# Performance work log

Hardware: AMD Instinct MI355X
Metric: run time of the kernel (lower is better)

Reference implementation:

```python
import jax, jax.numpy as jnp
import numpy as np

B, N_KV, N_Q = 32, 4096, 8
D_INP, D_SLOT, HEADS, MLP_H = 256, 256, 4, 1024
ITERS = 3
EPS = 1e-8


def _ln(x, g, b, eps=1e-5):
    m = jnp.mean(x, axis=-1, keepdims=True)
    v = jnp.var(x, axis=-1, keepdims=True)
    return (x - m) * jax.lax.rsqrt(v + eps) * g + b


def setup_inputs() -> dict:
    key = jax.random.key(0)
    ks = jax.random.split(key, 12)
    def w(k, shape, fan_in):
        return jax.random.normal(k, shape, jnp.float32) / np.float32(np.sqrt(fan_in))
    return {
        "inputs": jax.random.normal(ks[0], (B, N_KV, D_INP), jnp.float32),
        "slots": jax.random.normal(ks[1], (B, N_Q, D_SLOT), jnp.float32),
        "ln_in_g": jnp.ones((D_INP,), jnp.float32), "ln_in_b": jnp.zeros((D_INP,), jnp.float32),
        "ln_slot_g": jnp.ones((D_SLOT,), jnp.float32), "ln_slot_b": jnp.zeros((D_SLOT,), jnp.float32),
        "ln_mlp_g": jnp.ones((D_SLOT,), jnp.float32), "ln_mlp_b": jnp.zeros((D_SLOT,), jnp.float32),
        "Wq": w(ks[2], (D_SLOT, D_SLOT), D_SLOT),
        "Wk": w(ks[3], (D_SLOT, D_INP), D_INP),
        "Wv": w(ks[4], (D_SLOT, D_INP), D_INP),
        "W_ih": w(ks[5], (3 * D_SLOT, D_SLOT), D_SLOT),
        "W_hh": w(ks[6], (3 * D_SLOT, D_SLOT), D_SLOT),
        "b_ih": jnp.zeros((3 * D_SLOT,), jnp.float32),
        "b_hh": jnp.zeros((3 * D_SLOT,), jnp.float32),
        "W1": w(ks[7], (MLP_H, D_SLOT), D_SLOT), "b1": jnp.zeros((MLP_H,), jnp.float32),
        "W2": w(ks[8], (D_SLOT, MLP_H), MLP_H), "b2": jnp.zeros((D_SLOT,), jnp.float32),
    }


def reference(inputs, slots, ln_in_g, ln_in_b, ln_slot_g, ln_slot_b, ln_mlp_g, ln_mlp_b,
              Wq, Wk, Wv, W_ih, W_hh, b_ih, b_hh, W1, b1, W2, b2):
    Bb, Nkv, _ = inputs.shape
    _, Nq, Ds = slots.shape
    hd = Ds // HEADS

    x = _ln(inputs, ln_in_g, ln_in_b)
    # k, v: [B, H, N_kv, hd]; k pre-scaled by hd**-0.5 as in the original
    k = (x @ Wk.T).reshape(Bb, Nkv, HEADS, hd).transpose(0, 2, 1, 3) * (hd ** -0.5)
    v = (x @ Wv.T).reshape(Bb, Nkv, HEADS, hd).transpose(0, 2, 1, 3)

    attn_vis = attn_temp = None
    for it in range(ITERS):
        if it == ITERS - 1:
            slots = jax.lax.stop_gradient(slots)
        slots_prev = slots
        s = _ln(slots, ln_slot_g, ln_slot_b)
        q = (s @ Wq.T).reshape(Bb, Nq, HEADS, hd).transpose(0, 2, 1, 3)  # [B,H,Nq,hd]
        logits = jnp.einsum('bhnd,bhqd->bhnq', k, q)  # [B,H,Nkv,Nq]
        # competing softmax: normalize jointly over (head, slot) per input token
        lt = logits.transpose(0, 2, 1, 3).reshape(Bb, Nkv, HEADS * Nq)
        attn = jax.nn.softmax(lt, axis=-1).reshape(Bb, Nkv, HEADS, Nq).transpose(0, 2, 1, 3)
        attn_vis = attn.sum(axis=1)   # [B, Nkv, Nq]
        attn_temp = attn_vis          # original recomputes the identical softmax; same values
        a = attn + EPS
        a = a / a.sum(axis=-2, keepdims=True)  # renormalize over N_kv
        updates = jnp.einsum('bhnq,bhnd->bhqd', a, v).transpose(0, 2, 1, 3).reshape(Bb, Nq, Ds)
        # GRU cell (torch GRUCell math)
        gx = updates @ W_ih.T + b_ih
        gh = slots_prev @ W_hh.T + b_hh
        xr, xz, xn = jnp.split(gx, 3, axis=-1)
        hr, hz, hn = jnp.split(gh, 3, axis=-1)
        r = jax.nn.sigmoid(xr + hr)
        z = jax.nn.sigmoid(xz + hz)
        n = jnp.tanh(xn + r * hn)
        slots = (1.0 - z) * n + z * slots_prev
        # MLP with residual
        m = _ln(slots, ln_mlp_g, ln_mlp_b)
        slots = slots + (jax.nn.relu(m @ W1.T + b1) @ W2.T + b2)
    return slots, attn_vis, attn_temp
```

## Files before the change

kernel.cpp:

```cpp
#include <hip/hip_runtime.h>
#include <math.h>


#define NKV   4096
#define DD    256
#define HQN   32
#define EPSR  1e-8f

#define WS_V      0
#define WS_A0     262144
#define WS_A1     263168
#define WS_C0     264192
#define WS_C1     265216
#define WS_SLOTA  266240
#define WS_SLOTB  331776
#define WS_WQT    397312
#define WS_QF     462848
#define WS_WPGXH  528384
#define WS_WFT    921600
#define WS_WHHT   1314816
#define WS_W1T    1413120
#define WS_W2T    1544192
#define WS_RS     1675264
#define WS_RM     1806336
#define WS_VPART  1937408

typedef float f32x4 __attribute__((ext_vector_type(4)));
typedef short s16x8 __attribute__((ext_vector_type(8)));
typedef int   v2i   __attribute__((ext_vector_type(2)));

__device__ __forceinline__ unsigned bfr(float f) {
    unsigned u = __float_as_uint(f);
    return (u + 0x7fffu + ((u >> 16) & 1u)) >> 16;
}
__device__ __forceinline__ unsigned pk2(float lo, float hi) {
    return bfr(lo) | (bfr(hi) << 16);
}
__device__ __forceinline__ float bf2f(unsigned short us) {
    return __uint_as_float((unsigned)us << 16);
}
__device__ __forceinline__ float bflo(unsigned u) { return __uint_as_float(u << 16); }
__device__ __forceinline__ float bfhi(unsigned u) { return __uint_as_float(u & 0xffff0000u); }

__device__ __forceinline__ v2i tr_read(unsigned addr) {
    v2i d;
    asm volatile("ds_read_b64_tr_b16 %0, %1" : "=v"(d) : "v"(addr));
    return d;
}
__device__ __forceinline__ s16x8 mk_frag(v2i a, v2i b) {
    union { int i[4]; s16x8 s; } u;
    u.i[0] = a.x; u.i[1] = a.y; u.i[2] = b.x; u.i[3] = b.y;
    return u.s;
}

__global__ __launch_bounds__(256) void k_copy(const float* __restrict__ in,
                                              float* __restrict__ out, int n) {
    int i = blockIdx.x * 256 + threadIdx.x;
    if (i < n) out[i] = in[i];
}

__global__ __launch_bounds__(256) void k_tr(const float* __restrict__ in,
                                            float* __restrict__ out, int R, int C) {
    __shared__ float tile[32][33];
    int bx = blockIdx.x * 32, by = blockIdx.y * 32;
    int x = bx + threadIdx.x;
    for (int k = 0; k < 32; k += 8) {
        int y = by + threadIdx.y + k;
        if (x < C && y < R) tile[threadIdx.y + k][threadIdx.x] = in[(size_t)y * C + x];
    }
    __syncthreads();
    int r = by + threadIdx.x;
    for (int k = 0; k < 32; k += 8) {
        int c = bx + threadIdx.y + k;
        if (c < C && r < R) out[(size_t)c * R + r] = tile[threadIdx.x][threadIdx.y + k];
    }
}

__global__ __launch_bounds__(256) void k_wfold(
    const float* __restrict__ Wih, const float* __restrict__ Wv,
    unsigned* __restrict__ WfT2)
{
    __shared__ float wr[256];
    const int c = blockIdx.x, t = threadIdx.x;
    wr[t] = Wih[(size_t)c * 256 + t];
    __syncthreads();
    const float2* wv2 = (const float2*)Wv;
    #pragma unroll
    for (int pp = 0; pp < 2; ++pp) {
        int P = pp * 256 + t;
        int h = P >> 7, p = P & 127;
        float f0 = 0.f, f1 = 0.f;
        #pragma unroll 8
        for (int d = 0; d < 64; ++d) {
            float a = wr[h * 64 + d];
            float2 v = wv2[(size_t)(h * 64 + d) * 128 + p];
            f0 = fmaf(a, v.x, f0); f1 = fmaf(a, v.y, f1);
        }
        WfT2[(size_t)P * 768 + c] = pk2(f0, f1);
    }
}

__global__ __launch_bounds__(256) void k_trpack(
    const float* __restrict__ in, unsigned* __restrict__ out, int R, int C)
{
    const int c2 = blockIdx.x;
    const int t = threadIdx.x;
    for (int q = 0; q < R / 256; ++q) {
        int r = q * 256 + t;
        out[(size_t)c2 * R + r] = pk2(in[(size_t)r * C + 2 * c2],
                                      in[(size_t)r * C + 2 * c2 + 1]);
    }
}

__global__ __launch_bounds__(256) void k_prep_a(
    const float* __restrict__ slots, const float* __restrict__ g_s, const float* __restrict__ b_s,
    const float* __restrict__ wqt, float* __restrict__ qf_g,
    float* __restrict__ A0_g, float* __restrict__ A1_g)
{
    __shared__ float s_row[256];
    __shared__ float red[8];
    const int t = threadIdx.x;
    const int b = blockIdx.x, qi = blockIdx.y;
    const int lane = t & 63, w = t >> 6;

    if (t < 4) { A0_g[b * 32 + t * 8 + qi] = 0.f; A1_g[b * 32 + t * 8 + qi] = 0.f; }

    float v = slots[((size_t)b * 8 + qi) * 256 + t];
    float s0 = v, s1 = v * v;
    #pragma unroll
    for (int o = 32; o >= 1; o >>= 1) { s0 += __shfl_xor(s0, o, 64); s1 += __shfl_xor(s1, o, 64); }
    if (lane == 0) { red[w] = s0; red[4 + w] = s1; }
    __syncthreads();
    {
        float m = (red[0] + red[1] + red[2] + red[3]) * (1.f / 256.f);
        float q2 = (red[4] + red[5] + red[6] + red[7]) * (1.f / 256.f);
        float rs = rsqrtf(q2 - m * m + 1e-5f);
        s_row[t] = (v - m) * rs * g_s[t] + b_s[t];
    }
    __syncthreads();

    float a = 0.f;
    #pragma unroll 8
    for (int j = 0; j < 256; ++j)
        a = fmaf(s_row[j], wqt[j * 256 + t], a);
    qf_g[((size_t)b * 8 + qi) * 256 + t] = a;
}

__global__ __launch_bounds__(256) void k_prep_b(
    const float* __restrict__ qf_g, const float* __restrict__ Wk,
    const float* __restrict__ g_in, const float* __restrict__ b_in,
    unsigned short* __restrict__ wp_bf, float* __restrict__ c0_g, float* __restrict__ c1_g)
{
    __shared__ float qs[512];
    __shared__ float redc[4096];
    const int t = threadIdx.x;
    const int b = blockIdx.x, h = blockIdx.y;
    const int lane = t & 63, w = t >> 6;
    const float LNS = 0.125f * 1.44269504f;

    #pragma unroll
    for (int rep = 0; rep < 2; ++rep) {
        int idx = rep * 256 + t;
        int qi = idx >> 6, d = idx & 63;
        qs[idx] = qf_g[((size_t)b * 8 + qi) * 256 + h * 64 + d];
    }
    __syncthreads();

    float a2[8];
    #pragma unroll
    for (int qi = 0; qi < 8; ++qi) a2[qi] = 0.f;
    #pragma unroll 4
    for (int d = 0; d < 64; ++d) {
        float wv = Wk[(size_t)(h * 64 + d) * 256 + t];
        #pragma unroll
        for (int qi = 0; qi < 8; ++qi) a2[qi] = fmaf(qs[qi * 64 + d], wv, a2[qi]);
    }
    const float gv = g_in[t], bv = b_in[t];
    #pragma unroll
    for (int qi = 0; qi < 8; ++qi) {
        float kv = LNS * a2[qi];
        float we = kv * gv;
        wp_bf[((size_t)b * HQN + h * 8 + qi) * 256 + t] = (unsigned short)bfr(we);
        redc[qi * 256 + t] = we;
        redc[2048 + qi * 256 + t] = kv * bv;
    }
    __syncthreads();
    #pragma unroll
    for (int rep = 0; rep < 2; ++rep) {
        int r = w * 2 + rep;
        float sv1 = redc[r * 256 + lane] + redc[r * 256 + 64 + lane] +
                    redc[r * 256 + 128 + lane] + redc[r * 256 + 192 + lane];
        float sv0 = redc[2048 + r * 256 + lane] + redc[2048 + r * 256 + 64 + lane] +
                    redc[2048 + r * 256 + 128 + lane] + redc[2048 + r * 256 + 192 + lane];
        #pragma unroll
        for (int o = 32; o >= 1; o >>= 1) {
            sv1 += __shfl_xor(sv1, o, 64);
            sv0 += __shfl_xor(sv0, o, 64);
        }
        if (lane == 0) {
            c1_g[b * 32 + h * 8 + r] = sv1;
            c0_g[b * 32 + h * 8 + r] = sv0;
        }
    }
}

__device__ __forceinline__ void load_x(const float* __restrict__ inp, int b, int n0,
                                       int tok_s, int seg8, float4* ld) {
    const float4* row4 = (const float4*)(inp + ((size_t)b * NKV + n0 + tok_s) * 256);
    #pragma unroll
    for (int u = 0; u < 8; ++u) ld[u] = row4[(u >> 2) * 32 + seg8 * 4 + (u & 3)];
}

__device__ __forceinline__ void pack_x(const float4* ld, char* dst, int tok_s, int seg8) {
    #pragma unroll
    for (int c = 0; c < 2; ++c) {
        int nt = seg8 + 8 * c;
        #pragma unroll
        for (int h = 0; h < 2; ++h) {
            float4 fa = ld[c * 4 + h * 2], fb = ld[c * 4 + h * 2 + 1];
            uint4 pk;
            pk.x = pk2(fa.x, fa.y); pk.y = pk2(fa.z, fa.w);
            pk.z = pk2(fb.x, fb.y); pk.w = pk2(fb.z, fb.w);
            *(uint4*)(dst + nt * 1040 + tok_s * 32 + h * 16) = pk;
        }
    }
}

__device__ __forceinline__ void calc_stats(const float4* ld, float* sb,
                                           float* __restrict__ rs_g, float* __restrict__ rm_g,
                                           int b, int n0, int tok_s, int seg8) {
    float s0 = 0.f, s1 = 0.f;
    #pragma unroll
    for (int u = 0; u < 8; ++u) {
        float4 v = ld[u];
        s0 += v.x + v.y + v.z + v.w;
        s1 = fmaf(v.x, v.x, s1); s1 = fmaf(v.y, v.y, s1);
        s1 = fmaf(v.z, v.z, s1); s1 = fmaf(v.w, v.w, s1);
    }
    s0 += __shfl_xor(s0, 1, 64); s1 += __shfl_xor(s1, 1, 64);
    s0 += __shfl_xor(s0, 2, 64); s1 += __shfl_xor(s1, 2, 64);
    s0 += __shfl_xor(s0, 4, 64); s1 += __shfl_xor(s1, 4, 64);
    float m  = s0 * (1.f / 256.f);
    float rs = rsqrtf(s1 * (1.f / 256.f) - m * m + 1e-5f);
    if (seg8 == 0) {
        sb[tok_s] = rs;
        sb[32 + tok_s] = rs * m;
        rs_g[b * 4096 + n0 + tok_s] = rs;
        rm_g[b * 4096 + n0 + tok_s] = rs * m;
    }
}

template<int NC, int STATS, int WVIS>
__global__ __launch_bounds__(256) void k_attn(
    const float* __restrict__ inp, const unsigned short* __restrict__ wp_bf,
    const float* __restrict__ c0_g, const float* __restrict__ c1_g,
    float* __restrict__ vpart, float* __restrict__ A0_g, float* __restrict__ A1_g,
    float* __restrict__ rs_g, float* __restrict__ rm_g,
    float* __restrict__ out_vis, float* __restrict__ out_temp)
{
    constexpr int KBMAX = 128 / NC;
    __shared__ unsigned short xb[2][8320];
    __shared__ unsigned short wl[8192];
    __shared__ unsigned short pt[1024];
    __shared__ float stats[2][64];
    __shared__ float redm[64];
    __shared__ float reds[64];

    const int t = threadIdx.x;
    const int l = t & 63, w = t >> 6;
    const int g = l >> 4, li = l & 15;
    const int b = blockIdx.y, kb = blockIdx.x;

    char* xbB = (char*)xb;
    char* wlB = (char*)wl;
    char* ptB = (char*)pt;
    const int tok_s = t >> 3, seg8 = t & 7;
    const int cbase = kb * NC;

    {
        const uint4* wp4 = (const uint4*)wp_bf + ((size_t)b * 8192 + (t >> 3) * 256 + (t & 7) * 32) / 8;
        const int hq = t >> 3, sg = t & 7;
        #pragma unroll
        for (int q = 0; q < 4; ++q) {
            uint4 v = wp4[q];
            *(uint4*)(wlB + hq * 512 + (((sg * 4 + q) ^ (hq & 7)) * 16)) = v;
        }
    }

    const int Mt = w & 1, Nt = w >> 1;
    const int hqB = Nt * 16 + li;
    const float c0r = c0_g[b * 32 + hqB];
    const float c1r = c1_g[b * 32 + hqB];
    const int MtV = w >> 1, ntb = (w & 1) * 8;
    const int hqA = MtV * 16 + li;

    f32x4 av[8];
    #pragma unroll
    for (int u = 0; u < 8; ++u) av[u] = (f32x4){0.f, 0.f, 0.f, 0.f};
    float A0acc = 0.f, A1acc = 0.f;

    const unsigned xbase = (unsigned)(uintptr_t)xbB;

    {
        float4 ldA[8];
        load_x(inp, b, cbase * 32, tok_s, seg8, ldA);
        if (STATS) {
            calc_stats(ldA, &stats[0][0], rs_g, rm_g, b, cbase * 32, tok_s, seg8);
        } else {
            if (t < 32) stats[0][t] = rs_g[b * 4096 + cbase * 32 + t];
            else if (t < 64) stats[0][t] = rm_g[b * 4096 + cbase * 32 + t - 32];
        }
        pack_x(ldA, xbB, tok_s, seg8);
    }
    __syncthreads();

    #pragma unroll
    for (int ci = 0; ci < NC; ++ci) {
        const int cur = ci & 1, nxt = cur ^ 1;
        const int n0 = (cbase + ci) * 32;
        char* xc = xbB + cur * 16640;
        char* xn = xbB + nxt * 16640;

        float4 ldN[8];
        if (ci < NC - 1) load_x(inp, b, n0 + 32, tok_s, seg8, ldN);
        __builtin_amdgcn_sched_barrier(0);

        f32x4 accS = (f32x4){0.f, 0.f, 0.f, 0.f};
        #pragma unroll
        for (int kk = 0; kk < 8; ++kk) {
            s16x8 af = *(const s16x8*)(xc + (kk * 2 + (g >> 1)) * 1040 +
                                       (Mt * 16 + li) * 32 + (g & 1) * 16);
            s16x8 bf = *(const s16x8*)(wlB + hqB * 512 + (((kk * 4 + g) ^ (hqB & 7)) * 16));
            accS = __builtin_amdgcn_mfma_f32_16x16x32_bf16(af, bf, accS, 0, 0, 0);
        }

        float lg[4], rsv[4], rmv[4], mh[4], ex[4], aa[4];
        #pragma unroll
        for (int r = 0; r < 4; ++r) {
            int tokr = Mt * 16 + g * 4 + r;
            rsv[r] = stats[cur][tokr];
            rmv[r] = stats[cur][32 + tokr];
            lg[r] = fmaf(rsv[r], accS[r], fmaf(-rmv[r], c1r, c0r));
        }
        #pragma unroll
        for (int r = 0; r < 4; ++r) {
            float v = lg[r];
            v = fmaxf(v, __shfl_xor(v, 1, 64));
            v = fmaxf(v, __shfl_xor(v, 2, 64));
            v = fmaxf(v, __shfl_xor(v, 4, 64));
            v = fmaxf(v, __shfl_xor(v, 8, 64));
            mh[r] = v;
            ex[r] = exp2f(lg[r] - v);
            float s = ex[r];
            s += __shfl_xor(s, 1, 64);
            s += __shfl_xor(s, 2, 64);
            s += __shfl_xor(s, 4, 64);
            s += __shfl_xor(s, 8, 64);
            if (li == 0) {
                int tokr = Mt * 16 + g * 4 + r;
                redm[tokr * 2 + Nt] = v;
                reds[tokr * 2 + Nt] = s;
            }
        }
        __syncthreads();
        #pragma unroll
        for (int r = 0; r < 4; ++r) {
            int tokr = Mt * 16 + g * 4 + r;
            float m0 = redm[tokr * 2], m1 = redm[tokr * 2 + 1];
            float mx = fmaxf(m0, m1);
            float tot = reds[tokr * 2] * exp2f(m0 - mx) + reds[tokr * 2 + 1] * exp2f(m1 - mx);
            aa[r] = ex[r] * (exp2f(mh[r] - mx) / tot);
            A0acc += aa[r];
            A1acc = fmaf(aa[r], rmv[r], A1acc);
        }
        {
            uint2 pw;
            pw.x = pk2(aa[0] * rsv[0], aa[1] * rsv[1]);
            pw.y = pk2(aa[2] * rsv[2], aa[3] * rsv[3]);
            int tokb = Mt * 16 + g * 4;
            int slot = (tokb >> 3) ^ ((hqB >> 1) & 3);
            *(uint2*)(ptB + hqB * 64 + slot * 16 + (tokb & 7) * 2) = pw;
        }
        __syncthreads();

        if (WVIS) {
            int tk = t >> 3, q = t & 7;
            float sv = 0.f;
            #pragma unroll
            for (int h = 0; h < 4; ++h) {
                int hq = h * 8 + q;
                int slot = (tk >> 3) ^ ((hq >> 1) & 3);
                sv += bf2f(*(const unsigned short*)(ptB + hq * 64 + slot * 16 + (tk & 7) * 2));
            }
            float vv = sv / stats[cur][tk];
            size_t o = ((size_t)b * NKV + n0 + tk) * 8 + q;
            out_vis[o] = vv; out_temp[o] = vv;
        }

        if (ci < NC - 1) {
            if (STATS) {
                calc_stats(ldN, &stats[nxt][0], rs_g, rm_g, b, n0 + 32, tok_s, seg8);
            } else {
                if (t < 32) stats[nxt][t] = rs_g[b * 4096 + n0 + 32 + t];
                else if (t < 64) stats[nxt][t] = rm_g[b * 4096 + n0 + 32 + t - 32];
            }
            pack_x(ldN, xn, tok_s, seg8);
        }

        {
            s16x8 pa = *(const s16x8*)(ptB + hqA * 64 + ((g ^ ((hqA >> 1) & 3)) * 16));
            unsigned abase = xbase + cur * 16640 + g * 256 + li * 8;
            v2i t0a = tr_read(abase + (ntb + 0) * 1040);
            v2i t0b = tr_read(abase + (ntb + 0) * 1040 + 128);
            v2i t1a = tr_read(abase + (ntb + 1) * 1040);
            v2i t1b = tr_read(abase + (ntb + 1) * 1040 + 128);
            v2i t2a = tr_read(abase + (ntb + 2) * 1040);
            v2i t2b = tr_read(abase + (ntb + 2) * 1040 + 128);
            v2i t3a = tr_read(abase + (ntb + 3) * 1040);
            v2i t3b = tr_read(abase + (ntb + 3) * 1040 + 128);
            asm volatile("s_waitcnt lgkmcnt(0)" ::: "memory");
            __builtin_amdgcn_sched_barrier(0);
            av[0] = __builtin_amdgcn_mfma_f32_16x16x32_bf16(pa, mk_frag(t0a, t0b), av[0], 0, 0, 0);
            av[1] = __builtin_amdgcn_mfma_f32_16x16x32_bf16(pa, mk_frag(t1a, t1b), av[1], 0, 0, 0);
            av[2] = __builtin_amdgcn_mfma_f32_16x16x32_bf16(pa, mk_frag(t2a, t2b), av[2], 0, 0, 0);
            av[3] = __builtin_amdgcn_mfma_f32_16x16x32_bf16(pa, mk_frag(t3a, t3b), av[3], 0, 0, 0);
            v2i t4a = tr_read(abase + (ntb + 4) * 1040);
            v2i t4b = tr_read(abase + (ntb + 4) * 1040 + 128);
            v2i t5a = tr_read(abase + (ntb + 5) * 1040);
            v2i t5b = tr_read(abase + (ntb + 5) * 1040 + 128);
            v2i t6a = tr_read(abase + (ntb + 6) * 1040);
            v2i t6b = tr_read(abase + (ntb + 6) * 1040 + 128);
            v2i t7a = tr_read(abase + (ntb + 7) * 1040);
            v2i t7b = tr_read(abase + (ntb + 7) * 1040 + 128);
            asm volatile("s_waitcnt lgkmcnt(0)" ::: "memory");
            __builtin_amdgcn_sched_barrier(0);
            av[4] = __builtin_amdgcn_mfma_f32_16x16x32_bf16(pa, mk_frag(t4a, t4b), av[4], 0, 0, 0);
            av[5] = __builtin_amdgcn_mfma_f32_16x16x32_bf16(pa, mk_frag(t5a, t5b), av[5], 0, 0, 0);
            av[6] = __builtin_amdgcn_mfma_f32_16x16x32_bf16(pa, mk_frag(t6a, t6b), av[6], 0, 0, 0);
            av[7] = __builtin_amdgcn_mfma_f32_16x16x32_bf16(pa, mk_frag(t7a, t7b), av[7], 0, 0, 0);
        }
        __syncthreads();
    }

    A0acc += __shfl_xor(A0acc, 16, 64); A0acc += __shfl_xor(A0acc, 32, 64);
    A1acc += __shfl_xor(A1acc, 16, 64); A1acc += __shfl_xor(A1acc, 32, 64);
    if (g == 0) {
        atomicAdd(A0_g + b * 32 + hqB, A0acc);
        atomicAdd(A1_g + b * 32 + hqB, A1acc);
    }
    float* vp = vpart + ((size_t)(b * KBMAX + kb) * 32) * 256;
    #pragma unroll
    for (int i = 0; i < 8; ++i) {
        int j = (ntb + i) * 16 + li;
        #pragma unroll
        for (int r = 0; r < 4; ++r) {
            int hq = MtV * 16 + g * 4 + r;
            vp[(size_t)hq * 256 + j] = av[i][r];
        }
    }
}

template<int KBMAX>
__global__ __launch_bounds__(256) void k_vred(
    const float* __restrict__ vpart, float* __restrict__ V_g)
{
    const int t = threadIdx.x;
    const int b = blockIdx.x, hq = blockIdx.y;
    const float* p = vpart + ((size_t)(b * KBMAX) * 32 + hq) * 256 + t;
    float s = 0.f;
    #pragma unroll 8
    for (int kb = 0; kb < KBMAX; ++kb)
        s += p[(size_t)kb * 8192];
    V_g[((size_t)b * 32 + hq) * 256 + t] = s;
}

__global__ __launch_bounds__(256) void k_gates(
    const float* __restrict__ V_g, const float* __restrict__ A0_g,
    const float* __restrict__ A1_g,
    const float* __restrict__ g_in, const float* __restrict__ b_in,
    const float* __restrict__ slot_cur,
    const unsigned* __restrict__ WfT2, const unsigned* __restrict__ WhhT2,
    float* __restrict__ gxh, float* __restrict__ slot_nxt,
    float* __restrict__ out_slots)
{
    __shared__ __align__(16) float aT[1024 * 4];
    const int t = threadIdx.x;
    const int rg = blockIdx.y;
    const int chunk = blockIdx.x;
    const int row0 = rg * 4;
    float acc0 = 0.f, acc1 = 0.f, acc2 = 0.f, acc3 = 0.f;

    if (chunk == 0) {
        #pragma unroll
        for (int rr = 0; rr < 4; ++rr) {
            slot_nxt[(size_t)(row0 + rr) * 256 + t] = 0.f;
            if (out_slots) out_slots[(size_t)(row0 + rr) * 256 + t] = 0.f;
        }
    }

    if (chunk < 3) {
        const int b = rg >> 1, qi0 = (rg & 1) * 4;
        const float gt = g_in[t], bt = b_in[t];
        #pragma unroll
        for (int kk = 0; kk < 4; ++kk) {
            float4 y4;
            #pragma unroll
            for (int rr = 0; rr < 4; ++rr) {
                int hq = kk * 8 + qi0 + rr;
                float A0 = A0_g[b * 32 + hq], A1 = A1_g[b * 32 + hq];
                float den = A0 + EPSR * (float)NKV;
                float vv = V_g[((size_t)b * 32 + hq) * 256 + t];
                float yv = (gt * (vv - A1) + bt * A0) / den;
                ((float*)&y4)[rr] = yv;
            }
            *(float4*)(aT + (kk * 256 + t) * 4) = y4;
        }
        __syncthreads();
        const unsigned* wp = WfT2 + chunk * 256 + t;
        #pragma unroll 4
        for (int k2 = 0; k2 < 512; ++k2) {
            unsigned wv = wp[(size_t)k2 * 768];
            float w0 = bflo(wv), w1 = bfhi(wv);
            float4 a0 = *(const float4*)(aT + 8 * k2);
            float4 a1 = *(const float4*)(aT + 8 * k2 + 4);
            acc0 = fmaf(a0.x, w0, acc0); acc0 = fmaf(a1.x, w1, acc0);
            acc1 = fmaf(a0.y, w0, acc1); acc1 = fmaf(a1.y, w1, acc1);
            acc2 = fmaf(a0.z, w0, acc2); acc2 = fmaf(a1.z, w1, acc2);
            acc3 = fmaf(a0.w, w0, acc3); acc3 = fmaf(a1.w, w1, acc3);
        }
        float* go = gxh + (size_t)row0 * 1536 + chunk * 256 + t;
        go[0] = acc0; go[1536] = acc1; go[3072] = acc2; go[4608] = acc3;
    } else {
        const int gc = chunk - 3;
        {
            float4 y4;
            #pragma unroll
            for (int rr = 0; rr < 4; ++rr)
                ((float*)&y4)[rr] = slot_cur[(size_t)(row0 + rr) * 256 + t];
            *(float4*)(aT + t * 4) = y4;
        }
        __syncthreads();
        const unsigned* wp = WhhT2 + gc * 256 + t;
        #pragma unroll 4
        for (int k2 = 0; k2 < 128; ++k2) {
            unsigned wv = wp[(size_t)k2 * 768];
            float w0 = bflo(wv), w1 = bfhi(wv);
            float4 a0 = *(const float4*)(aT + 8 * k2);
            float4 a1 = *(const float4*)(aT + 8 * k2 + 4);
            acc0 = fmaf(a0.x, w0, acc0); acc0 = fmaf(a1.x, w1, acc0);
            acc1 = fmaf(a0.y, w0, acc1); acc1 = fmaf(a1.y, w1, acc1);
            acc2 = fmaf(a0.z, w0, acc2); acc2 = fmaf(a1.z, w1, acc2);
            acc3 = fmaf(a0.w, w0, acc3); acc3 = fmaf(a1.w, w1, acc3);
        }
        float* go = gxh + (size_t)row0 * 1536 + 768 + gc * 256 + t;
        go[0] = acc0; go[1536] = acc1; go[3072] = acc2; go[4608] = acc3;
    }
}

__global__ __launch_bounds__(256) void k_mlp(
    const float* __restrict__ gxh, const float* __restrict__ slot_cur,
    const float* __restrict__ bih, const float* __restrict__ bhh,
    const float* __restrict__ gm, const float* __restrict__ bm,
    const unsigned* __restrict__ W1T2, const float* __restrict__ b1,
    const unsigned* __restrict__ W2T2, const float* __restrict__ b2,
    float* __restrict__ slot_nxt, float* __restrict__ out_slots)
{
    __shared__ __align__(16) float mT[1024];
    __shared__ float sm_l[4][256];
    __shared__ float h1_l[4][256];
    __shared__ float lnst[8];
    const int t = threadIdx.x;
    const int rg = blockIdx.y, chunk = blockIdx.x;
    const int row0 = rg * 4;
    const int lane = t & 63, w = t >> 6;

    const float bi0 = bih[t], bi1 = bih[256 + t], bi2 = bih[512 + t];
    const float bh0 = bhh[t], bh1 = bhh[256 + t], bh2 = bhh[512 + t];
    float smid[4];
    #pragma unroll
    for (int rr = 0; rr < 4; ++rr) {
        const float* gr = gxh + (size_t)(row0 + rr) * 1536;
        float gx0 = gr[t], gx1 = gr[256 + t], gx2 = gr[512 + t];
        float gh0 = gr[768 + t], gh1 = gr[1024 + t], gh2 = gr[1280 + t];
        float spv = slot_cur[(size_t)(row0 + rr) * 256 + t];
        float r = 1.f / (1.f + __expf(-(gx0 + bi0 + gh0 + bh0)));
        float z = 1.f / (1.f + __expf(-(gx1 + bi1 + gh1 + bh1)));
        float n = tanhf(gx2 + bi2 + r * (gh2 + bh2));
        smid[rr] = (1.f - z) * n + z * spv;
        sm_l[rr][t] = smid[rr];
    }
    __syncthreads();
    {
        float4 v = *(const float4*)(&sm_l[w][lane * 4]);
        float s0 = v.x + v.y + v.z + v.w;
        float s1 = v.x * v.x + v.y * v.y + v.z * v.z + v.w * v.w;
        #pragma unroll
        for (int o = 32; o >= 1; o >>= 1) { s0 += __shfl_xor(s0, o, 64); s1 += __shfl_xor(s1, o, 64); }
        if (lane == 0) {
            float mu = s0 * (1.f / 256.f);
            lnst[w * 2] = mu;
            lnst[w * 2 + 1] = rsqrtf(s1 * (1.f / 256.f) - mu * mu + 1e-5f);
        }
    }
    __syncthreads();
    {
        const float gmt = gm[t], bmt = bm[t];
        float4 m4;
        #pragma unroll
        for (int rr = 0; rr < 4; ++rr)
            ((float*)&m4)[rr] = (smid[rr] - lnst[rr * 2]) * lnst[rr * 2 + 1] * gmt + bmt;
        *(float4*)(mT + t * 4) = m4;
    }
    __syncthreads();

    {
        float acc0 = 0.f, acc1 = 0.f, acc2 = 0.f, acc3 = 0.f;
        const unsigned* wp = W1T2 + chunk * 256 + t;
        #pragma unroll 4
        for (int k2 = 0; k2 < 128; ++k2) {
            unsigned wv = wp[(size_t)k2 * 1024];
            float w0 = bflo(wv), w1 = bfhi(wv);
            float4 a0 = *(const float4*)(mT + 8 * k2);
            float4 a1 = *(const float4*)(mT + 8 * k2 + 4);
            acc0 = fmaf(a0.x, w0, acc0); acc0 = fmaf(a1.x, w1, acc0);
            acc1 = fmaf(a0.y, w0, acc1); acc1 = fmaf(a1.y, w1, acc1);
            acc2 = fmaf(a0.z, w0, acc2); acc2 = fmaf(a1.z, w1, acc2);
            acc3 = fmaf(a0.w, w0, acc3); acc3 = fmaf(a1.w, w1, acc3);
        }
        const float b1t = b1[chunk * 256 + t];
        h1_l[0][t] = fmaxf(acc0 + b1t, 0.f);
        h1_l[1][t] = fmaxf(acc1 + b1t, 0.f);
        h1_l[2][t] = fmaxf(acc2 + b1t, 0.f);
        h1_l[3][t] = fmaxf(acc3 + b1t, 0.f);
    }
    __syncthreads();

    {
        float o0 = 0.f, o1 = 0.f, o2 = 0.f, o3 = 0.f;
        const unsigned* wp = W2T2 + (size_t)(chunk * 128) * 256 + t;
        #pragma unroll 4
        for (int k2 = 0; k2 < 128; ++k2) {
            unsigned wv = wp[(size_t)k2 * 256];
            float w0 = bflo(wv), w1 = bfhi(wv);
            float a00 = h1_l[0][2 * k2], a01 = h1_l[0][2 * k2 + 1];
            float a10 = h1_l[1][2 * k2], a11 = h1_l[1][2 * k2 + 1];
            float a20 = h1_l[2][2 * k2], a21 = h1_l[2][2 * k2 + 1];
            float a30 = h1_l[3][2 * k2], a31 = h1_l[3][2 * k2 + 1];
            o0 = fmaf(a00, w0, o0); o0 = fmaf(a01, w1, o0);
            o1 = fmaf(a10, w0, o1); o1 = fmaf(a11, w1, o1);
            o2 = fmaf(a20, w0, o2); o2 = fmaf(a21, w1, o2);
            o3 = fmaf(a30, w0, o3); o3 = fmaf(a31, w1, o3);
        }
        const float b2t = b2[t];
        float p0 = o0 + ((chunk == 0) ? smid[0] + b2t : 0.f);
        float p1 = o1 + ((chunk == 0) ? smid[1] + b2t : 0.f);
        float p2 = o2 + ((chunk == 0) ? smid[2] + b2t : 0.f);
        float p3 = o3 + ((chunk == 0) ? smid[3] + b2t : 0.f);
        atomicAdd(slot_nxt + (size_t)(row0 + 0) * 256 + t, p0);
        atomicAdd(slot_nxt + (size_t)(row0 + 1) * 256 + t, p1);
        atomicAdd(slot_nxt + (size_t)(row0 + 2) * 256 + t, p2);
        atomicAdd(slot_nxt + (size_t)(row0 + 3) * 256 + t, p3);
        if (out_slots) {
            atomicAdd(out_slots + (size_t)(row0 + 0) * 256 + t, p0);
            atomicAdd(out_slots + (size_t)(row0 + 1) * 256 + t, p1);
            atomicAdd(out_slots + (size_t)(row0 + 2) * 256 + t, p2);
            atomicAdd(out_slots + (size_t)(row0 + 3) * 256 + t, p3);
        }
    }
}

extern "C" void kernel_launch(void* const* d_in, const int* in_sizes, int n_in,
                              void* d_out, int out_size, void* d_ws, size_t ws_size,
                              hipStream_t stream) {
    const float* inp     = (const float*)d_in[0];
    const float* slots0  = (const float*)d_in[1];
    const float* ln_in_g = (const float*)d_in[2];
    const float* ln_in_b = (const float*)d_in[3];
    const float* ln_s_g  = (const float*)d_in[4];
    const float* ln_s_b  = (const float*)d_in[5];
    const float* ln_m_g  = (const float*)d_in[6];
    const float* ln_m_b  = (const float*)d_in[7];
    const float* Wq  = (const float*)d_in[8];
    const float* Wk  = (const float*)d_in[9];
    const float* Wv  = (const float*)d_in[10];
    const float* Wih = (const float*)d_in[11];
    const float* Whh = (const float*)d_in[12];
    const float* bih = (const float*)d_in[13];
    const float* bhh = (const float*)d_in[14];
    const float* W1  = (const float*)d_in[15];
    const float* b1  = (const float*)d_in[16];
    const float* W2  = (const float*)d_in[17];
    const float* b2  = (const float*)d_in[18];

    float* ws = (float*)d_ws;
    float* V_g   = ws + WS_V;
    float* A0_g  = ws + WS_A0;
    float* A1_g  = ws + WS_A1;
    float* c0_g  = ws + WS_C0;
    float* c1_g  = ws + WS_C1;
    float* slotA = ws + WS_SLOTA;
    float* slotB = ws + WS_SLOTB;
    float* wqt   = ws + WS_WQT;
    float* qf_g  = ws + WS_QF;
    float* gxh   = ws + WS_WPGXH;
    unsigned short* wp_bf = (unsigned short*)(ws + WS_WPGXH);
    unsigned* WfT2  = (unsigned*)(ws + WS_WFT);
    unsigned* WhhT2 = (unsigned*)(ws + WS_WHHT);
    unsigned* W1T2  = (unsigned*)(ws + WS_W1T);
    unsigned* W2T2  = (unsigned*)(ws + WS_W2T);
    float* rs_g  = ws + WS_RS;
    float* rm_g  = ws + WS_RM;
    float* vpart = ws + WS_VPART;

    const int useNC2 = (ws_size >= (size_t)(WS_VPART + 32ull * 64 * 8192) * 4) ? 1 : 0;

    float* out_slots = (float*)d_out;
    float* out_vis   = out_slots + 32 * 8 * 256;
    float* out_temp  = out_vis + 32 * 4096 * 8;

    k_tr<<<dim3(8, 8), dim3(32, 8), 0, stream>>>(Wq, wqt, 256, 256);
    k_wfold<<<768, 256, 0, stream>>>(Wih, Wv, WfT2);
    k_trpack<<<128, 256, 0, stream>>>(Whh, WhhT2, 768, 256);
    k_trpack<<<128, 256, 0, stream>>>(W1, W1T2, 1024, 256);
    k_trpack<<<512, 256, 0, stream>>>(W2, W2T2, 256, 1024);
    k_copy<<<256, 256, 0, stream>>>(slots0, slotA, 65536);

    for (int it = 0; it < 3; ++it) {
        float* cur = (it & 1) ? slotB : slotA;
        float* nxt = (it & 1) ? slotA : slotB;
        k_prep_a<<<dim3(32, 8), 256, 0, stream>>>(cur, ln_s_g, ln_s_b, wqt, qf_g,
                                                  A0_g, A1_g);
        k_prep_b<<<dim3(32, 4), 256, 0, stream>>>(qf_g, Wk, ln_in_g, ln_in_b,
                                                  wp_bf, c0_g, c1_g);
        if (useNC2) {
            if (it == 0)
                k_attn<2, 1, 0><<<dim3(64, 32), 256, 0, stream>>>(
                    inp, wp_bf, c0_g, c1_g, vpart, A0_g, A1_g, rs_g, rm_g, out_vis, out_temp);
            else if (it == 1)
                k_attn<2, 0, 0><<<dim3(64, 32), 256, 0, stream>>>(
                    inp, wp_bf, c0_g, c1_g, vpart, A0_g, A1_g, rs_g, rm_g, out_vis, out_temp);
            else
                k_attn<2, 0, 1><<<dim3(64, 32), 256, 0, stream>>>(
                    inp, wp_bf, c0_g, c1_g, vpart, A0_g, A1_g, rs_g, rm_g, out_vis, out_temp);
            k_vred<64><<<dim3(32, 32), 256, 0, stream>>>(vpart, V_g);
        } else {
            if (it == 0)
                k_attn<4, 1, 0><<<dim3(32, 32), 256, 0, stream>>>(
                    inp, wp_bf, c0_g, c1_g, vpart, A0_g, A1_g, rs_g, rm_g, out_vis, out_temp);
            else if (it == 1)
                k_attn<4, 0, 0><<<dim3(32, 32), 256, 0, stream>>>(
                    inp, wp_bf, c0_g, c1_g, vpart, A0_g, A1_g, rs_g, rm_g, out_vis, out_temp);
            else
                k_attn<4, 0, 1><<<dim3(32, 32), 256, 0, stream>>>(
                    inp, wp_bf, c0_g, c1_g, vpart, A0_g, A1_g, rs_g, rm_g, out_vis, out_temp);
            k_vred<32><<<dim3(32, 32), 256, 0, stream>>>(vpart, V_g);
        }
        k_gates<<<dim3(6, 64), 256, 0, stream>>>(
            V_g, A0_g, A1_g, ln_in_g, ln_in_b, cur, WfT2, WhhT2, gxh, nxt,
            (it == 2) ? out_slots : nullptr);
        k_mlp<<<dim3(4, 64), 256, 0, stream>>>(
            gxh, cur, bih, bhh, ln_m_g, ln_m_b, W1T2, b1, W2T2, b2, nxt,
            (it == 2) ? out_slots : nullptr);
    }
}
```

Baseline: 474.3 us.

## Fuse prep kernels, single-buffer x tile, store V partials as bf16

Merges the two per-iteration prep kernels into one, so the slot LayerNorm and the Wq projection are computed in LDS and the q intermediate is never written to or read from global memory. The attention kernel drops the double-buffered x tile for a single buffer, with an extra barrier before repacking, which halves that LDS footprint and may raise occupancy but serialises the load and compute overlap. V partial sums are now written as packed bf16 pairs and reduced in fp32 by k_vred, halving partial-sum traffic at the cost of precision. The NC=2 path is now always used and no longer depends on workspace size.

```diff
diff --git a/kernel.cpp b/kernel.cpp
--- a/kernel.cpp
+++ b/kernel.cpp
@@ -15,15 +15,14 @@
 #define WS_SLOTA  266240
 #define WS_SLOTB  331776
 #define WS_WQT    397312
-#define WS_QF     462848
-#define WS_WPGXH  528384
-#define WS_WFT    921600
-#define WS_WHHT   1314816
-#define WS_W1T    1413120
-#define WS_W2T    1544192
-#define WS_RS     1675264
-#define WS_RM     1806336
-#define WS_VPART  1937408
+#define WS_WPGXH  462848
+#define WS_WFT    856064
+#define WS_WHHT   1249280
+#define WS_W1T    1347584
+#define WS_W2T    1478656
+#define WS_RS     1609728
+#define WS_RM     1740800
+#define WS_VPART  1871872
 
 typedef float f32x4 __attribute__((ext_vector_type(4)));
 typedef short s16x8 __attribute__((ext_vector_type(8)));
@@ -112,45 +111,14 @@
     }
 }
 
-__global__ __launch_bounds__(256) void k_prep_a(
+__global__ __launch_bounds__(256) void k_prep(
     const float* __restrict__ slots, const float* __restrict__ g_s, const float* __restrict__ b_s,
-    const float* __restrict__ wqt, float* __restrict__ qf_g,
+    const float* __restrict__ wqt, const float* __restrict__ Wk,
+    const float* __restrict__ g_in, const float* __restrict__ b_in,
+    unsigned short* __restrict__ wp_bf, float* __restrict__ c0_g, float* __restrict__ c1_g,
     float* __restrict__ A0_g, float* __restrict__ A1_g)
 {
-    __shared__ float s_row[256];
-    __shared__ float red[8];
-    const int t = threadIdx.x;
-    const int b = blockIdx.x, qi = blockIdx.y;
-    const int lane = t & 63, w = t >> 6;
-
-    if (t < 4) { A0_g[b * 32 + t * 8 + qi] = 0.f; A1_g[b * 32 + t * 8 + qi] = 0.f; }
-
-    float v = slots[((size_t)b * 8 + qi) * 256 + t];
-    float s0 = v, s1 = v * v;
-    #pragma unroll
-    for (int o = 32; o >= 1; o >>= 1) { s0 += __shfl_xor(s0, o, 64); s1 += __shfl_xor(s1, o, 64); }
-    if (lane == 0) { red[w] = s0; red[4 + w] = s1; }
-    __syncthreads();
-    {
-        float m = (red[0] + red[1] + red[2] + red[3]) * (1.f / 256.f);
-        float q2 = (red[4] + red[5] + red[6] + red[7]) * (1.f / 256.f);
-        float rs = rsqrtf(q2 - m * m + 1e-5f);
-        s_row[t] = (v - m) * rs * g_s[t] + b_s[t];
-    }
-    __syncthreads();
-
-    float a = 0.f;
-    #pragma unroll 8
-    for (int j = 0; j < 256; ++j)
-        a = fmaf(s_row[j], wqt[j * 256 + t], a);
-    qf_g[((size_t)b * 8 + qi) * 256 + t] = a;
-}
-
-__global__ __launch_bounds__(256) void k_prep_b(
-    const float* __restrict__ qf_g, const float* __restrict__ Wk,
-    const float* __restrict__ g_in, const float* __restrict__ b_in,
-    unsigned short* __restrict__ wp_bf, float* __restrict__ c0_g, float* __restrict__ c1_g)
-{
+    __shared__ float s_lds[2048];
     __shared__ float qs[512];
     __shared__ float redc[4096];
     const int t = threadIdx.x;
@@ -158,11 +126,38 @@
     const int lane = t & 63, w = t >> 6;
     const float LNS = 0.125f * 1.44269504f;
 
-    #pragma unroll
-    for (int rep = 0; rep < 2; ++rep) {
-        int idx = rep * 256 + t;
-        int qi = idx >> 6, d = idx & 63;
-        qs[idx] = qf_g[((size_t)b * 8 + qi) * 256 + h * 64 + d];
+    if (h == 0 && t < 32) { A0_g[b * 32 + t] = 0.f; A1_g[b * 32 + t] = 0.f; }
+
+    for (int r = w; r < 8; r += 4) {
+        const float4 v = ((const float4*)(slots + ((size_t)b * 8 + r) * 256))[lane];
+        float s0 = v.x + v.y + v.z + v.w;
+        float s1 = v.x * v.x + v.y * v.y + v.z * v.z + v.w * v.w;
+        #pragma unroll
+        for (int o = 32; o >= 1; o >>= 1) { s0 += __shfl_xor(s0, o, 64); s1 += __shfl_xor(s1, o, 64); }
+        float m = s0 * (1.f / 256.f);
+        float rs = rsqrtf(s1 * (1.f / 256.f) - m * m + 1e-5f);
+        float4 gg = ((const float4*)g_s)[lane];
+        float4 bb = ((const float4*)b_s)[lane];
+        float4 nn;
+        nn.x = (v.x - m) * rs * gg.x + bb.x;
+        nn.y = (v.y - m) * rs * gg.y + bb.y;
+        nn.z = (v.z - m) * rs * gg.z + bb.z;
+        nn.w = (v.w - m) * rs * gg.w + bb.w;
+        ((float4*)(s_lds + r * 256))[lane] = nn;
+    }
+    __syncthreads();
+
+    {
+        const int qi0 = t >> 6, d = t & 63;
+        float a0 = 0.f, a1 = 0.f;
+        #pragma unroll 8
+        for (int j = 0; j < 256; ++j) {
+            float wv = wqt[j * 256 + h * 64 + d];
+            a0 = fmaf(s_lds[qi0 * 256 + j], wv, a0);
+            a1 = fmaf(s_lds[(qi0 + 4) * 256 + j], wv, a1);
+        }
+        qs[qi0 * 64 + d] = a0;
+        qs[(qi0 + 4) * 64 + d] = a1;
     }
     __syncthreads();
 
@@ -254,12 +249,12 @@
 __global__ __launch_bounds__(256) void k_attn(
     const float* __restrict__ inp, const unsigned short* __restrict__ wp_bf,
     const float* __restrict__ c0_g, const float* __restrict__ c1_g,
-    float* __restrict__ vpart, float* __restrict__ A0_g, float* __restrict__ A1_g,
+    unsigned* __restrict__ vpart, float* __restrict__ A0_g, float* __restrict__ A1_g,
     float* __restrict__ rs_g, float* __restrict__ rm_g,
     float* __restrict__ out_vis, float* __restrict__ out_temp)
 {
     constexpr int KBMAX = 128 / NC;
-    __shared__ unsigned short xb[2][8320];
+    __shared__ unsigned short xb[8320];
     __shared__ unsigned short wl[8192];
     __shared__ unsigned short pt[1024];
     __shared__ float stats[2][64];
@@ -318,8 +313,6 @@
     for (int ci = 0; ci < NC; ++ci) {
         const int cur = ci & 1, nxt = cur ^ 1;
         const int n0 = (cbase + ci) * 32;
-        char* xc = xbB + cur * 16640;
-        char* xn = xbB + nxt * 16640;
 
         float4 ldN[8];
         if (ci < NC - 1) load_x(inp, b, n0 + 32, tok_s, seg8, ldN);
@@ -328,7 +321,7 @@
         f32x4 accS = (f32x4){0.f, 0.f, 0.f, 0.f};
         #pragma unroll
         for (int kk = 0; kk < 8; ++kk) {
-            s16x8 af = *(const s16x8*)(xc + (kk * 2 + (g >> 1)) * 1040 +
+            s16x8 af = *(const s16x8*)(xbB + (kk * 2 + (g >> 1)) * 1040 +
                                        (Mt * 16 + li) * 32 + (g & 1) * 16);
             s16x8 bf = *(const s16x8*)(wlB + hqB * 512 + (((kk * 4 + g) ^ (hqB & 7)) * 16));
             accS = __builtin_amdgcn_mfma_f32_16x16x32_bf16(af, bf, accS, 0, 0, 0);
@@ -404,12 +397,11 @@
                 if (t < 32) stats[nxt][t] = rs_g[b * 4096 + n0 + 32 + t];
                 else if (t < 64) stats[nxt][t] = rm_g[b * 4096 + n0 + 32 + t - 32];
             }
-            pack_x(ldN, xn, tok_s, seg8);
         }
 
         {
             s16x8 pa = *(const s16x8*)(ptB + hqA * 64 + ((g ^ ((hqA >> 1) & 3)) * 16));
-            unsigned abase = xbase + cur * 16640 + g * 256 + li * 8;
+            unsigned abase = xbase + g * 256 + li * 8;
             v2i t0a = tr_read(abase + (ntb + 0) * 1040);
             v2i t0b = tr_read(abase + (ntb + 0) * 1040 + 128);
             v2i t1a = tr_read(abase + (ntb + 1) * 1040);
@@ -440,6 +432,11 @@
             av[7] = __builtin_amdgcn_mfma_f32_16x16x32_bf16(pa, mk_frag(t7a, t7b), av[7], 0, 0, 0);
         }
         __syncthreads();
+
+        if (ci < NC - 1) {
+            pack_x(ldN, xbB, tok_s, seg8);
+            __syncthreads();
+        }
     }
 
     A0acc += __shfl_xor(A0acc, 16, 64); A0acc += __shfl_xor(A0acc, 32, 64);
@@ -448,30 +445,41 @@
         atomicAdd(A0_g + b * 32 + hqB, A0acc);
         atomicAdd(A1_g + b * 32 + hqB, A1acc);
     }
-    float* vp = vpart + ((size_t)(b * KBMAX + kb) * 32) * 256;
-    #pragma unroll
-    for (int i = 0; i < 8; ++i) {
-        int j = (ntb + i) * 16 + li;
+    {
+        const size_t blk = (size_t)b * KBMAX + kb;
         #pragma unroll
         for (int r = 0; r < 4; ++r) {
             int hq = MtV * 16 + g * 4 + r;
-            vp[(size_t)hq * 256 + j] = av[i][r];
+            unsigned* vp = vpart + (blk * 32 + hq) * 128 + li;
+            #pragma unroll
+            for (int ip = 0; ip < 4; ++ip) {
+                unsigned u = pk2(av[2 * ip][r], av[2 * ip + 1][r]);
+                int jp = (ntb >> 1) + ip;
+                vp[jp * 16] = u;
+            }
         }
     }
 }
 
 template<int KBMAX>
 __global__ __launch_bounds__(256) void k_vred(
-    const float* __restrict__ vpart, float* __restrict__ V_g)
+    const unsigned* __restrict__ vpart, float* __restrict__ V_g)
 {
     const int t = threadIdx.x;
-    const int b = blockIdx.x, hq = blockIdx.y;
-    const float* p = vpart + ((size_t)(b * KBMAX) * 32 + hq) * 256 + t;
-    float s = 0.f;
+    const int b = blockIdx.x;
+    const int hq = blockIdx.y * 2 + (t >> 7);
+    const int tl = t & 127;
+    const unsigned* p = vpart + ((size_t)(b * KBMAX) * 32 + hq) * 128 + tl;
+    float lo = 0.f, hi = 0.f;
     #pragma unroll 8
-    for (int kb = 0; kb < KBMAX; ++kb)
-        s += p[(size_t)kb * 8192];
-    V_g[((size_t)b * 32 + hq) * 256 + t] = s;
+    for (int kb = 0; kb < KBMAX; ++kb) {
+        unsigned u = p[(size_t)kb * 4096];
+        lo += bflo(u); hi += bfhi(u);
+    }
+    const int jp = tl >> 4, li = tl & 15;
+    float* vo = V_g + ((size_t)b * 32 + hq) * 256 + jp * 32 + li;
+    vo[0]  = lo;
+    vo[16] = hi;
 }
 
 __global__ __launch_bounds__(256) void k_gates(
@@ -701,7 +709,6 @@
     float* slotA = ws + WS_SLOTA;
     float* slotB = ws + WS_SLOTB;
     float* wqt   = ws + WS_WQT;
-    float* qf_g  = ws + WS_QF;
     float* gxh   = ws + WS_WPGXH;
     unsigned short* wp_bf = (unsigned short*)(ws + WS_WPGXH);
     unsigned* WfT2  = (unsigned*)(ws + WS_WFT);
@@ -710,9 +717,7 @@
     unsigned* W2T2  = (unsigned*)(ws + WS_W2T);
     float* rs_g  = ws + WS_RS;
     float* rm_g  = ws + WS_RM;
-    float* vpart = ws + WS_VPART;
-
-    const int useNC2 = (ws_size >= (size_t)(WS_VPART + 32ull * 64 * 8192) * 4) ? 1 : 0;
+    unsigned* vpart = (unsigned*)(ws + WS_VPART);
 
     float* out_slots = (float*)d_out;
     float* out_vis   = out_slots + 32 * 8 * 256;
@@ -728,33 +733,19 @@
     for (int it = 0; it < 3; ++it) {
         float* cur = (it & 1) ? slotB : slotA;
         float* nxt = (it & 1) ? slotA : slotB;
-        k_prep_a<<<dim3(32, 8), 256, 0, stream>>>(cur, ln_s_g, ln_s_b, wqt, qf_g,
-                                                  A0_g, A1_g);
-        k_prep_b<<<dim3(32, 4), 256, 0, stream>>>(qf_g, Wk, ln_in_g, ln_in_b,
-                                                  wp_bf, c0_g, c1_g);
-        if (useNC2) {
-            if (it == 0)
-                k_attn<2, 1, 0><<<dim3(64, 32), 256, 0, stream>>>(
-                    inp, wp_bf, c0_g, c1_g, vpart, A0_g, A1_g, rs_g, rm_g, out_vis, out_temp);
-            else if (it == 1)
-                k_attn<2, 0, 0><<<dim3(64, 32), 256, 0, stream>>>(
-                    inp, wp_bf, c0_g, c1_g, vpart, A0_g, A1_g, rs_g, rm_g, out_vis, out_temp);
-            else
-                k_attn<2, 0, 1><<<dim3(64, 32), 256, 0, stream>>>(
-                    inp, wp_bf, c0_g, c1_g, vpart, A0_g, A1_g, rs_g, rm_g, out_vis, out_temp);
-            k_vred<64><<<dim3(32, 32), 256, 0, stream>>>(vpart, V_g);
-        } else {
-            if (it == 0)
-                k_attn<4, 1, 0><<<dim3(32, 32), 256, 0, stream>>>(
-                    inp, wp_bf, c0_g, c1_g, vpart, A0_g, A1_g, rs_g, rm_g, out_vis, out_temp);
-            else if (it == 1)
-                k_attn<4, 0, 0><<<dim3(32, 32), 256, 0, stream>>>(
-                    inp, wp_bf, c0_g, c1_g, vpart, A0_g, A1_g, rs_g, rm_g, out_vis, out_temp);
-            else
-                k_attn<4, 0, 1><<<dim3(32, 32), 256, 0, stream>>>(
-                    inp, wp_bf, c0_g, c1_g, vpart, A0_g, A1_g, rs_g, rm_g, out_vis, out_temp);
-            k_vred<32><<<dim3(32, 32), 256, 0, stream>>>(vpart, V_g);
-        }
+        k_prep<<<dim3(32, 4), 256, 0, stream>>>(cur, ln_s_g, ln_s_b, wqt, Wk,
+                                                ln_in_g, ln_in_b, wp_bf,
+                                                c0_g, c1_g, A0_g, A1_g);
+        if (it == 0)
+            k_attn<2, 1, 0><<<dim3(64, 32), 256, 0, stream>>>(
+                inp, wp_bf, c0_g, c1_g, vpart, A0_g, A1_g, rs_g, rm_g, out_vis, out_temp);
+        else if (it == 1)
+            k_attn<2, 0, 0><<<dim3(64, 32), 256, 0, stream>>>(
+                inp, wp_bf, c0_g, c1_g, vpart, A0_g, A1_g, rs_g, rm_g, out_vis, out_temp);
+        else
+            k_attn<2, 0, 1><<<dim3(64, 32), 256, 0, stream>>>(
+                inp, wp_bf, c0_g, c1_g, vpart, A0_g, A1_g, rs_g, rm_g, out_vis, out_temp);
+        k_vred<64><<<dim3(32, 16), 256, 0, stream>>>(vpart, V_g);
         k_gates<<<dim3(6, 64), 256, 0, stream>>>(
             V_g, A0_g, A1_g, ln_in_g, ln_in_b, cur, WfT2, WhhT2, gxh, nxt,
             (it == 2) ? out_slots : nullptr);
```

New measurement: 452.9 us. 1.05x faster.
